# Kernel tuning notes

Hardware: AMD Instinct MI355X
Metric: run time of the kernel (lower is better)

The kernel has to match this reference:

```python
import jax, jax.numpy as jnp
import numpy as np
import math

E = 768      # embed_dim
N = 16       # ssm state_dim
K = 4        # d_conv
R = 48       # dt_rank = ceil(E/16)
DEPTH = 4
V = 32000    # vocab
B = 2
L = 1024
T = 100
H = 4 * E    # mlp hidden


def layer_norm(x, g, b):
    mu = jnp.mean(x, axis=-1, keepdims=True)
    var = jnp.mean(jnp.square(x - mu), axis=-1, keepdims=True)
    return (x - mu) * jax.lax.rsqrt(var + 1e-5) * g + b


def sin_emb(t, dim):
    half = dim // 2
    freqs = jnp.exp(-math.log(10000.0) * jnp.arange(half, dtype=jnp.float32) / half)
    args = t.astype(jnp.float32)[:, None] * freqs
    return jnp.concatenate([jnp.sin(args), jnp.cos(args)], axis=-1)


def ssm_forward(x, z_w, p_w, conv_w, dtp_w, dtp_b, A_log, Dp, out_w):
    # x: (B, L, E)
    z = x @ z_w.T
    params = x @ p_w.T                      # (B, L, R+2N)
    dt_un, _B_unused, Cp = jnp.split(params, [R, R + N], axis=-1)
    dt = jax.nn.softplus(dt_un @ dtp_w.T + dtp_b)   # (B, L, E)
    # depthwise causal conv (torch pads both sides d_conv-1 then trims -> left pad only)
    xc = jax.lax.conv_general_dilated(
        jnp.transpose(x, (0, 2, 1)), conv_w, (1,), [(K - 1, 0)],
        feature_group_count=E, dimension_numbers=('NCH', 'OIH', 'NCH'))
    u = jax.nn.silu(jnp.transpose(xc, (0, 2, 1)))   # (B, L, E)
    A = -jnp.exp(A_log)                              # (E, N)
    A_t = jnp.exp(dt[..., None] * A)                 # (B, L, E, N)
    B_t = jnp.where(jnp.abs(A) < 1e-5, dt[..., None], (A_t - 1.0) / (A + 1e-10))
    # recurrence exactly as source: h[0]=B[0]*u[0]; h[t]=A[t-1]*h[t-1]+B[t-1]*u[t-1]
    h0 = B_t[:, 0] * u[:, 0, :, None]                # (B, E, N)
    xs = (jnp.moveaxis(A_t[:, :-1], 1, 0),
          jnp.moveaxis(B_t[:, :-1], 1, 0),
          jnp.moveaxis(u[:, :-1], 1, 0))
    def step(h, inp):
        a, b, uu = inp
        h = a * h + b * uu[..., None]
        return h, h
    _, hs = jax.lax.scan(step, h0, xs)               # (L-1, B, E, N)
    h_all = jnp.concatenate([h0[None], hs], axis=0)  # (L, B, E, N)
    y = jnp.einsum('bln,lben->ble', Cp, h_all)
    y = y + u * Dp
    return (y * jax.nn.silu(z)) @ out_w.T


def setup_inputs() -> dict:
    key = jax.random.key(0)
    ks = list(jax.random.split(key, 32))
    it = iter(ks)
    def nrm(shape, fan_in):
        return jax.random.normal(next(it), shape, jnp.float32) * np.sqrt(2.0 / fan_in)
    d = {}
    d['tokens'] = jax.random.randint(next(it), (B, L), 0, V + 1)
    d['timesteps'] = jax.random.randint(next(it), (B,), 0, T)
    d['tok_emb'] = jax.random.normal(next(it), (V + 1, E), jnp.float32) * 0.02
    d['time_w1'] = nrm((H, E), E); d['time_b1'] = jnp.zeros((H,), jnp.float32)
    d['time_w2'] = nrm((E, H), H); d['time_b2'] = jnp.zeros((E,), jnp.float32)
    d['ln1_g'] = jnp.ones((DEPTH, E), jnp.float32); d['ln1_b'] = jnp.zeros((DEPTH, E), jnp.float32)
    d['z_w'] = nrm((DEPTH, E, E), E)
    d['p_w'] = nrm((DEPTH, R + 2 * N, E), E)
    d['conv_w'] = jax.random.normal(next(it), (DEPTH, E, 1, K), jnp.float32) * np.sqrt(1.0 / K)
    s = R ** -0.5 * 0.1
    d['dtp_w'] = jax.random.uniform(next(it), (DEPTH, E, R), jnp.float32, -s, s)
    d['dtp_b'] = jnp.full((DEPTH, E), math.log(math.expm1(0.001)), jnp.float32)
    d['A_log'] = jnp.tile(jnp.log(jnp.arange(1, N + 1, dtype=jnp.float32)), (DEPTH, E, 1))
    d['D_param'] = jnp.ones((DEPTH, E), jnp.float32)
    d['out_w'] = nrm((DEPTH, E, E), E)
    d['ln2_g'] = jnp.ones((DEPTH, E), jnp.float32); d['ln2_b'] = jnp.zeros((DEPTH, E), jnp.float32)
    d['mlp_w1'] = nrm((DEPTH, H, E), E); d['mlp_b1'] = jnp.zeros((DEPTH, H), jnp.float32)
    d['mlp_w2'] = nrm((DEPTH, E, H), H); d['mlp_b2'] = jnp.zeros((DEPTH, E), jnp.float32)
    d['lnout_g'] = jnp.ones((E,), jnp.float32); d['lnout_b'] = jnp.zeros((E,), jnp.float32)
    d['head_w'] = nrm((V, E), E); d['head_b'] = jnp.zeros((V,), jnp.float32)
    return d


def reference(tokens, timesteps, tok_emb, time_w1, time_b1, time_w2, time_b2,
              ln1_g, ln1_b, z_w, p_w, conv_w, dtp_w, dtp_b, A_log, D_param, out_w,
              ln2_g, ln2_b, mlp_w1, mlp_b1, mlp_w2, mlp_b2,
              lnout_g, lnout_b, head_w, head_b):
    temb = sin_emb(timesteps, E)
    temb = jax.nn.silu(temb @ time_w1.T + time_b1) @ time_w2.T + time_b2
    x = tok_emb[tokens] + temb[:, None, :]           # (B, L, E)
    for i in range(DEPTH):
        x = x + ssm_forward(layer_norm(x, ln1_g[i], ln1_b[i]),
                            z_w[i], p_w[i], conv_w[i], dtp_w[i], dtp_b[i],
                            A_log[i], D_param[i], out_w[i])
        h = layer_norm(x, ln2_g[i], ln2_b[i])
        h = jax.nn.gelu(h @ mlp_w1[i].T + mlp_b1[i], approximate=False) @ mlp_w2[i].T + mlp_b2[i]
        x = x + h
    x = layer_norm(x, lnout_g, lnout_b)
    return x @ head_w.T + head_b                     # (B, L, V)
```

## Files before the change

kernel.cpp:

```cpp
#include <hip/hip_runtime.h>
#include <math.h>

#define EE 768
#define NS 16
#define RR 48
#define NDEPTH 4
#define NB 2
#define NL 1024
#define NH 3072
#define NV 32000
#define M_ROWS (NB*NL)
#define NC 64
#define CL 16
#define ZPW 896
#define LOG2E 1.44269504088896f
#define LN2   0.69314718055995f

typedef __attribute__((ext_vector_type(8))) __bf16 bf16x8;
typedef __attribute__((ext_vector_type(4))) __bf16 bf16x4;
typedef __attribute__((ext_vector_type(4))) float f32x4;

__device__ __forceinline__ void gl_lds16(const __bf16* g, __bf16* l){
  __builtin_amdgcn_global_load_lds(
      (const __attribute__((address_space(1))) void*)g,
      (__attribute__((address_space(3))) void*)l, 16, 0, 0);
}

enum { BE_STORE=0, BE_BIAS=1, BE_RESID=2, BE_BIAS_RESID=3, BE_BIAS_GELU_B16=4,
       BE_STORE_ZP=5 };

template<int EPI, int BMT, int BNT>
__global__ __launch_bounds__(256) void gemm_bf16(const __bf16* __restrict__ A,
    const __bf16* __restrict__ W, const float* __restrict__ bias,
    void* __restrict__ Cv, float* __restrict__ dtf, float* __restrict__ aux,
    int N, int K, int gx, int gy)
{
  const int nwg = gx*gy;
  const int orig = blockIdx.x;
  const int q = nwg >> 3, r = nwg & 7;
  const int xcd = orig & 7, bse = orig >> 3;
  int wg = (xcd < r ? xcd*(q+1) : r*(q+1) + (xcd-r)*q) + bse;
  const int GN = 16;
  const int per = gy*GN;
  const int g = wg / per;
  const int gstart = g*GN;
  const int gw0 = gx - gstart;
  const int gw = (GN < gw0) ? GN : gw0;
  const int local = wg - g*per;
  const int bx = gstart + local % gw;
  const int by = local / gw;

  constexpr int MFR = BMT/32;
  constexpr int NFR = BNT/32;
  __shared__ __bf16 As[BMT][64];
  __shared__ __bf16 Ws[BNT][64];
  const int bm = by*BMT, bn = bx*BNT;
  const int tid = threadIdx.x;
  const int w = tid>>6, lane = tid&63;
  const int wr = w>>1, wc = w&1;
  const int fr = lane&15, kg = lane>>4;
  const int sr8 = lane>>3;
  const int sg  = lane&7;
  const int ksrc = ((sg ^ sr8) & 7)*8;

  f32x4 acc[MFR][NFR];
  #pragma unroll
  for (int m=0;m<MFR;m++)
    #pragma unroll
    for (int n=0;n<NFR;n++)
      acc[m][n] = (f32x4){0.f,0.f,0.f,0.f};

  for (int k0=0;k0<K;k0+=64){
    const __bf16* gA = A + (size_t)(bm + w*(BMT/4) + sr8)*K + k0 + ksrc;
    #pragma unroll
    for (int c8=0;c8<BMT/32;c8++)
      gl_lds16(gA + (size_t)(c8*8)*K, &As[w*(BMT/4) + c8*8][0]);
    const __bf16* gW = W + (size_t)(bn + w*(BNT/4) + sr8)*K + k0 + ksrc;
    #pragma unroll
    for (int c8=0;c8<BNT/32;c8++)
      gl_lds16(gW + (size_t)(c8*8)*K, &Ws[w*(BNT/4) + c8*8][0]);
    __syncthreads();
    #pragma unroll
    for (int kk=0;kk<2;kk++){
      const int sp = (((kg + kk*4) ^ (fr&7)) & 7) * 8;
      bf16x8 af[MFR], bfr[NFR];
      #pragma unroll
      for (int m=0;m<MFR;m++) af[m]  = *(const bf16x8*)&As[wr*(BMT/2) + m*16 + fr][sp];
      #pragma unroll
      for (int n=0;n<NFR;n++) bfr[n] = *(const bf16x8*)&Ws[wc*(BNT/2) + n*16 + fr][sp];
      #pragma unroll
      for (int m=0;m<MFR;m++)
        #pragma unroll
        for (int n=0;n<NFR;n++)
          acc[m][n] = __builtin_amdgcn_mfma_f32_16x16x32_bf16(af[m], bfr[n], acc[m][n], 0,0,0);
    }
    __syncthreads();
  }

  float* Cf = (float*)Cv;
  __bf16* Cb = (__bf16*)Cv;
  #pragma unroll
  for (int m=0;m<MFR;m++){
    int row = bm + wr*(BMT/2) + m*16 + kg*4;
    #pragma unroll
    for (int n=0;n<NFR;n++){
      int col = bn + wc*(BNT/2) + n*16 + fr;
      float bsv = 0.f;
      if (EPI==BE_BIAS || EPI==BE_BIAS_RESID || EPI==BE_BIAS_GELU_B16)
        bsv = bias[col];
      #pragma unroll
      for (int rr2=0;rr2<4;rr2++){
        float v = acc[m][n][rr2];
        size_t idx = (size_t)(row+rr2)*N + col;
        if (EPI==BE_STORE)            Cf[idx] = v;
        else if (EPI==BE_BIAS)        Cf[idx] = v + bsv;
        else if (EPI==BE_RESID)       Cf[idx] += v;
        else if (EPI==BE_BIAS_RESID)  Cf[idx] += v + bsv;
        else if (EPI==BE_BIAS_GELU_B16){
          float xg = v + bsv; Cb[idx] = (__bf16)(0.5f*xg*(1.f+erff(xg*0.70710678118654752f)));
        } else if (EPI==BE_STORE_ZP){
          if (col < 768)                    Cb[(size_t)(row+rr2)*EE + col] = (__bf16)v;
          else if (col < 816)               dtf[(size_t)(row+rr2)*RR + (col-768)] = v;
          else if (col >= 832 && col < 848) aux[(size_t)(row+rr2)*16 + (col-832)] = v;
        }
      }
    }
  }
}

__global__ __launch_bounds__(512) void gemm_head256(const __bf16* __restrict__ A,
    const __bf16* __restrict__ W, const float* __restrict__ bias,
    float* __restrict__ C)
{
  const int gx = NV/256, gy = M_ROWS/256;
  const int nwg = gx*gy;
  const int orig = blockIdx.x;
  const int q = nwg >> 3;
  const int xcd = orig & 7, bse = orig >> 3;
  int wg = xcd*q + bse;
  const int GN = 8;
  const int per = gy*GN;
  const int g = wg / per;
  const int gstart = g*GN;
  const int gw0 = gx - gstart;
  const int gw = (GN < gw0) ? GN : gw0;
  const int local = wg - g*per;
  const int bx = gstart + local % gw;
  const int by = local / gw;

  __shared__ __bf16 Ah[2][256][64];
  __shared__ __bf16 Wh[2][256][64];
  const int bm = by*256, bn = bx*256;
  const int tid = threadIdx.x;
  const int w = tid>>6, lane = tid&63;
  const int wr = w>>2, wc = w&3;
  const int fr = lane&15, kg = lane>>4;
  const int ksrc = (((lane&7) ^ ((lane>>3)&7)) & 7)*8;

  f32x4 acc[8][4];
  #pragma unroll
  for (int m=0;m<8;m++)
    #pragma unroll
    for (int n=0;n<4;n++)
      acc[m][n] = (f32x4){0.f,0.f,0.f,0.f};

  auto stage = [&](int bufp, int kt){
    const __bf16* gA = A + (size_t)(bm + w*8 + (lane>>3))*EE + kt*64 + ksrc;
    #pragma unroll
    for (int j=0;j<4;j++)
      gl_lds16(gA + (size_t)(j*64)*EE, &Ah[bufp][j*64 + w*8][0]);
    const __bf16* gW = W + (size_t)(bn + w*8 + (lane>>3))*EE + kt*64 + ksrc;
    #pragma unroll
    for (int j=0;j<4;j++)
      gl_lds16(gW + (size_t)(j*64)*EE, &Wh[bufp][j*64 + w*8][0]);
  };

  auto compute = [&](int bufp){
    bf16x8 bfr[4][2];
    #pragma unroll
    for (int kk=0;kk<2;kk++){
      const int sp = (((kg + kk*4) ^ (fr&7)) & 7) * 8;
      #pragma unroll
      for (int n=0;n<4;n++)
        bfr[n][kk] = *(const bf16x8*)&Wh[bufp][wc*64 + n*16 + fr][sp];
    }
    #pragma unroll
    for (int m=0;m<8;m++){
      const int arow = wr*128 + m*16 + fr;
      const int sp0 = ((kg ^ (fr&7)) & 7) * 8;
      const int sp1 = (((kg+4) ^ (fr&7)) & 7) * 8;
      bf16x8 a0 = *(const bf16x8*)&Ah[bufp][arow][sp0];
      bf16x8 a1 = *(const bf16x8*)&Ah[bufp][arow][sp1];
      #pragma unroll
      for (int n=0;n<4;n++){
        acc[m][n] = __builtin_amdgcn_mfma_f32_16x16x32_bf16(a0, bfr[n][0], acc[m][n], 0,0,0);
        acc[m][n] = __builtin_amdgcn_mfma_f32_16x16x32_bf16(a1, bfr[n][1], acc[m][n], 0,0,0);
      }
    }
  };

  stage(0, 0);
  __syncthreads();
  for (int kt=0; kt<12; kt+=2){
    stage(1, kt+1);
    compute(0);
    __syncthreads();
    if (kt+2 < 12) stage(0, kt+2);
    compute(1);
    __syncthreads();
  }

  #pragma unroll
  for (int m=0;m<8;m++){
    int row = bm + wr*128 + m*16 + kg*4;
    #pragma unroll
    for (int n=0;n<4;n++){
      int col = bn + wc*64 + n*16 + fr;
      float bsv = bias[col];
      #pragma unroll
      for (int rr2=0;rr2<4;rr2++)
        C[(size_t)(row+rr2)*NV + col] = acc[m][n][rr2] + bsv;
    }
  }
}

#define S1E 2752512LL
#define S2E 5111808LL
#define S3E 14548992LL
#define S4E 23986176LL
#define STOT 48562176LL

__global__ void f2b_all(const float* __restrict__ zw, const float* __restrict__ pw,
                        const float* __restrict__ ow, const float* __restrict__ m1,
                        const float* __restrict__ m2, const float* __restrict__ hw,
                        __bf16* __restrict__ o){
  long long idx = ((long long)blockIdx.x*256 + threadIdx.x)*4;
  if (idx >= STOT) return;
  float4 v;
  if (idx < S1E){
    long long layer = idx / (ZPW*EE);
    int rem = (int)(idx - layer*(ZPW*EE));
    int row = rem / EE, col = rem - (rem/EE)*EE;
    if (row < 768)      v = *(const float4*)(zw + ((size_t)layer*EE + row)*EE + col);
    else if (row < 848) v = *(const float4*)(pw + ((size_t)layer*80 + (row-768))*EE + col);
    else                v = make_float4(0.f,0.f,0.f,0.f);
  }
  else if (idx < S2E) v = *(const float4*)(ow + (idx - S1E));
  else if (idx < S3E) v = *(const float4*)(m1 + (idx - S2E));
  else if (idx < S4E) v = *(const float4*)(m2 + (idx - S3E));
  else                v = *(const float4*)(hw + (idx - S4E));
  bf16x4 rb = { (__bf16)v.x, (__bf16)v.y, (__bf16)v.z, (__bf16)v.w };
  *(bf16x4*)(o+idx) = rb;
}

__global__ __launch_bounds__(256) void ln_kernel(const float* __restrict__ x,
    const float* __restrict__ gp, const float* __restrict__ bp, __bf16* __restrict__ yb)
{
  int row = blockIdx.x*4 + (threadIdx.x>>6);
  int lane = threadIdx.x & 63;
  const float* xr = x + (size_t)row*EE;
  float4 v0 = *(const float4*)(xr + lane*4);
  float4 v1 = *(const float4*)(xr + 256 + lane*4);
  float4 v2 = *(const float4*)(xr + 512 + lane*4);
  float s = (v0.x+v0.y)+(v0.z+v0.w) + (v1.x+v1.y)+(v1.z+v1.w) + (v2.x+v2.y)+(v2.z+v2.w);
  float q = v0.x*v0.x+v0.y*v0.y+v0.z*v0.z+v0.w*v0.w
          + v1.x*v1.x+v1.y*v1.y+v1.z*v1.z+v1.w*v1.w
          + v2.x*v2.x+v2.y*v2.y+v2.z*v2.z+v2.w*v2.w;
  #pragma unroll
  for (int m=1;m<64;m<<=1){ s += __shfl_xor(s, m, 64); q += __shfl_xor(q, m, 64); }
  float mu  = s*(1.f/768.f);
  float var = q*(1.f/768.f) - mu*mu;
  float inv = 1.0f/sqrtf(var + 1e-5f);
  __bf16* ybr = yb + (size_t)row*EE;
  #pragma unroll
  for (int p=0;p<3;p++){
    const float4 v = (p==0)? v0 : (p==1)? v1 : v2;
    int o = p*256 + lane*4;
    float4 gg = *(const float4*)(gp + o);
    float4 bb = *(const float4*)(bp + o);
    bf16x4 ov = { (__bf16)((v.x-mu)*inv*gg.x + bb.x),
                  (__bf16)((v.y-mu)*inv*gg.y + bb.y),
                  (__bf16)((v.z-mu)*inv*gg.z + bb.z),
                  (__bf16)((v.w-mu)*inv*gg.w + bb.w) };
    *(bf16x4*)(ybr + o) = ov;
  }
}

__global__ void sinemb_kernel(const int* __restrict__ timesteps, float* __restrict__ emb){
  int i = blockIdx.x*256+threadIdx.x;
  if (i >= NB*EE) return;
  int b = i/EE, e = i - b*EE;
  int half = EE/2;
  int j = (e<half)? e : e-half;
  float freq = expf(-logf(10000.f)*(float)j/(float)half);
  float arg = (float)timesteps[b]*freq;
  emb[i] = (e<half)? sinf(arg) : cosf(arg);
}

__global__ void time_mlp1(const float* __restrict__ emb, const float* __restrict__ w1,
                          const float* __restrict__ b1, float* __restrict__ thid){
  int wid = (blockIdx.x*256 + threadIdx.x)>>6;
  int lane = threadIdx.x & 63;
  int b = wid / NH, h = wid - b*NH;
  const float* er = emb + b*EE;
  const float* wr = w1 + (size_t)h*EE;
  float s = 0.f;
  #pragma unroll
  for (int j=0;j<EE/64;j++) s = fmaf(er[j*64+lane], wr[j*64+lane], s);
  #pragma unroll
  for (int m=1;m<64;m<<=1) s += __shfl_xor(s, m, 64);
  if (lane==0){
    s += b1[h];
    thid[wid] = s/(1.f+expf(-s));
  }
}

__global__ void time_mlp2(const float* __restrict__ thid, const float* __restrict__ w2,
                          const float* __restrict__ b2, float* __restrict__ temb){
  int wid = (blockIdx.x*256 + threadIdx.x)>>6;
  int lane = threadIdx.x & 63;
  int b = wid / EE, e = wid - b*EE;
  const float* tr = thid + b*NH;
  const float* wr = w2 + (size_t)e*NH;
  float s = 0.f;
  #pragma unroll
  for (int j=0;j<NH/64;j++) s = fmaf(tr[j*64+lane], wr[j*64+lane], s);
  #pragma unroll
  for (int m=1;m<64;m<<=1) s += __shfl_xor(s, m, 64);
  if (lane==0) temb[wid] = s + b2[e];
}

__global__ void embed_kernel(const int* __restrict__ tokens, const float* __restrict__ tok_emb,
                             const float* __restrict__ temb, float* __restrict__ x){
  int idx = blockIdx.x*256+threadIdx.x;
  int e = idx % EE; int bl = idx / EE; int b = bl / NL;
  int tok = tokens[bl];
  x[idx] = tok_emb[(size_t)tok*EE + e] + temb[b*EE + e];
}

__device__ __forceinline__ float dot48(const float* __restrict__ row, const float* wdf){
  float a0=0.f,a1=0.f,a2=0.f,a3=0.f;
  #pragma unroll
  for (int j=0;j<12;j++){
    float4 v = *(const float4*)(row + j*4);
    a0 = fmaf(v.x, wdf[j*4+0], a0);
    a1 = fmaf(v.y, wdf[j*4+1], a1);
    a2 = fmaf(v.z, wdf[j*4+2], a2);
    a3 = fmaf(v.w, wdf[j*4+3], a3);
  }
  return (a0+a1)+(a2+a3);
}
__device__ __forceinline__ float softplus_f(float x){
  return fmaxf(x,0.f) + LN2*log2f(1.f + exp2f(-LOG2E*fabsf(x)));
}
__device__ __forceinline__ float silu_f(float x){
  return x/(1.f + exp2f(-LOG2E*x));
}

__global__ __launch_bounds__(256) void scan_fused(
    const __bf16* __restrict__ xnb, const float* __restrict__ dtun,
    const float* __restrict__ dtw, const float* __restrict__ dtbias,
    const float* __restrict__ cwp, const float* __restrict__ A_log,
    const float* __restrict__ Dp, const float* __restrict__ cpf,
    const __bf16* __restrict__ zgb, __bf16* __restrict__ gb)
{
  __shared__ float Pl[NC][4][NS];
  __shared__ float Sl[NC][4][NS];
  __shared__ float dtc_l[CL][256];
  __shared__ float uc_l[CL+1][256];
  const int tid = threadIdx.x;
  const int e_l = tid & 3, c = tid >> 2;
  const int b  = blockIdx.x / (EE/4);
  const int eg = blockIdx.x % (EE/4);
  const int e  = eg*4 + e_l;

  float wdf[48];
  #pragma unroll
  for (int j=0;j<12;j++){
    float4 v = *(const float4*)(dtw + (size_t)e*RR + j*4);
    wdf[j*4]=v.x; wdf[j*4+1]=v.y; wdf[j*4+2]=v.z; wdf[j*4+3]=v.w;
  }
  float4 cw = *(const float4*)(cwp + e*4);
  float bias = dtbias[e];
  float Dv = Dp[e];
  float Av2[NS], iAv[NS];
  #pragma unroll
  for (int n4=0;n4<4;n4++){
    float4 v = *(const float4*)(A_log + (size_t)e*NS + n4*4);
    float a0=-exp2f(LOG2E*v.x), a1=-exp2f(LOG2E*v.y), a2=-exp2f(LOG2E*v.z), a3=-exp2f(LOG2E*v.w);
    Av2[n4*4+0]=a0*LOG2E; Av2[n4*4+1]=a1*LOG2E; Av2[n4*4+2]=a2*LOG2E; Av2[n4*4+3]=a3*LOG2E;
    iAv[n4*4+0]=1.f/(a0+1e-10f); iAv[n4*4+1]=1.f/(a1+1e-10f);
    iAv[n4*4+2]=1.f/(a2+1e-10f); iAv[n4*4+3]=1.f/(a3+1e-10f);
  }
  const __bf16* xcol = xnb + (size_t)b*NL*EE + e;
  const float* dtrow0 = dtun + (size_t)b*NL*RR;
  const int cs = c*CL;

  {
    float xw0,xw1,xw2,xw3;
    int prow = (c==0)? 0 : cs-1;
    xw0 = (prow-3>=0)? (float)xcol[(size_t)(prow-3)*EE] : 0.f;
    xw1 = (prow-2>=0)? (float)xcol[(size_t)(prow-2)*EE] : 0.f;
    xw2 = (prow-1>=0)? (float)xcol[(size_t)(prow-1)*EE] : 0.f;
    xw3 = (float)xcol[(size_t)prow*EE];
    float up  = silu_f(cw.x*xw0 + cw.y*xw1 + cw.z*xw2 + cw.w*xw3);
    float dtp_ = softplus_f(dot48(dtrow0 + (size_t)prow*RR, wdf) + bias);
    float h[NS];
    float sumdt = 0.f;
    #pragma unroll
    for (int n=0;n<NS;n++) h[n]=0.f;
    for (int i=0;i<CL;i++){
      int tt = cs+i;
      bool z0 = (tt==0);
      dtc_l[i][tid] = dtp_;
      uc_l[i][tid]  = up;
      sumdt += dtp_;
      #pragma unroll
      for (int n=0;n<NS;n++){
        float at = exp2f(dtp_*Av2[n]);
        float bt = (at-1.f)*iAv[n];
        float s = bt*up;
        h[n] = z0 ? s : fmaf(at, h[n], s);
      }
      if (tt>0){
        xw0=xw1; xw1=xw2; xw2=xw3; xw3 = (float)xcol[(size_t)tt*EE];
        up  = silu_f(cw.x*xw0 + cw.y*xw1 + cw.z*xw2 + cw.w*xw3);
        dtp_ = softplus_f(dot48(dtrow0 + (size_t)tt*RR, wdf) + bias);
      }
    }
    uc_l[CL][tid] = up;
    #pragma unroll
    for (int n4=0;n4<4;n4++){
      float4 pv;
      if (c==0) pv = make_float4(0.f,0.f,0.f,0.f);
      else pv = make_float4(exp2f(Av2[n4*4+0]*sumdt), exp2f(Av2[n4*4+1]*sumdt),
                            exp2f(Av2[n4*4+2]*sumdt), exp2f(Av2[n4*4+3]*sumdt));
      *(float4*)&Pl[c][e_l][n4*4] = pv;
      *(float4*)&Sl[c][e_l][n4*4] = make_float4(h[n4*4],h[n4*4+1],h[n4*4+2],h[n4*4+3]);
    }
  }
  __syncthreads();
  if (tid < 64){
    int el2 = tid & 3, n = tid >> 2;
    float hh = 0.f;
    for (int cc=0; cc<NC; cc++){
      float pp = Pl[cc][el2][n], ss = Sl[cc][el2][n];
      Pl[cc][el2][n] = hh;
      hh = fmaf(pp, hh, ss);
    }
  }
  __syncthreads();
  {
    float h[NS];
    #pragma unroll
    for (int n4=0;n4<4;n4++){
      float4 v = *(const float4*)&Pl[c][e_l][n4*4];
      h[n4*4]=v.x; h[n4*4+1]=v.y; h[n4*4+2]=v.z; h[n4*4+3]=v.w;
    }
    #pragma unroll
    for (int i=0;i<CL;i++){
      int tt = cs+i;
      bool z0 = (tt==0);
      float dtp_ = dtc_l[i][tid];
      float up   = uc_l[i][tid];
      float ucur = uc_l[i+1][tid];
      #pragma unroll
      for (int n=0;n<NS;n++){
        float at = exp2f(dtp_*Av2[n]);
        float bt = (at-1.f)*iAv[n];
        float s = bt*up;
        h[n] = z0 ? s : fmaf(at, h[n], s);
      }
      const float* cpr = cpf + (size_t)(b*NL+tt)*16;
      float y = 0.f;
      #pragma unroll
      for (int n4=0;n4<4;n4++){
        float4 cv = *(const float4*)(cpr + n4*4);
        y = fmaf(cv.x, h[n4*4], y);   y = fmaf(cv.y, h[n4*4+1], y);
        y = fmaf(cv.z, h[n4*4+2], y); y = fmaf(cv.w, h[n4*4+3], y);
      }
      float zv = (float)zgb[(size_t)(b*NL+tt)*EE + e];
      gb[(size_t)(b*NL+tt)*EE + e] = (__bf16)((y + ucur*Dv)*silu_f(zv));
    }
  }
}

extern "C" void kernel_launch(void* const* d_in, const int* in_sizes, int n_in,
                              void* d_out, int out_size, void* d_ws, size_t ws_size,
                              hipStream_t stream) {
  const int*   tokens    = (const int*)d_in[0];
  const int*   timesteps = (const int*)d_in[1];
  const float* tok_emb   = (const float*)d_in[2];
  const float* time_w1   = (const float*)d_in[3];
  const float* time_b1   = (const float*)d_in[4];
  const float* time_w2   = (const float*)d_in[5];
  const float* time_b2   = (const float*)d_in[6];
  const float* ln1_g     = (const float*)d_in[7];
  const float* ln1_b     = (const float*)d_in[8];
  const float* z_w       = (const float*)d_in[9];
  const float* p_w       = (const float*)d_in[10];
  const float* conv_w    = (const float*)d_in[11];
  const float* dtp_w     = (const float*)d_in[12];
  const float* dtp_b     = (const float*)d_in[13];
  const float* A_log     = (const float*)d_in[14];
  const float* D_param   = (const float*)d_in[15];
  const float* out_w     = (const float*)d_in[16];
  const float* ln2_g     = (const float*)d_in[17];
  const float* ln2_b     = (const float*)d_in[18];
  const float* mlp_w1    = (const float*)d_in[19];
  const float* mlp_b1    = (const float*)d_in[20];
  const float* mlp_w2    = (const float*)d_in[21];
  const float* mlp_b2    = (const float*)d_in[22];
  const float* lnout_g   = (const float*)d_in[23];
  const float* lnout_b   = (const float*)d_in[24];
  const float* head_w    = (const float*)d_in[25];
  const float* head_b    = (const float*)d_in[26];
  float* out = (float*)d_out;

  float* ws = (float*)d_ws;
  float* x      = ws;
  float* cpf    = x    + (size_t)M_ROWS*EE;
  float* dtun   = cpf  + (size_t)M_ROWS*16;
  float* emb    = dtun + (size_t)M_ROWS*RR;
  float* thid   = emb + NB*EE;
  __bf16* xnb   = (__bf16*)(thid + NB*NH);
  __bf16* zgb   = xnb + (size_t)M_ROWS*EE;
  __bf16* gb    = zgb + (size_t)M_ROWS*EE;
  __bf16* hidb  = gb  + (size_t)M_ROWS*EE;
  __bf16* wzp   = hidb + (size_t)M_ROWS*NH;
  __bf16* wout  = wzp  + (size_t)NDEPTH*ZPW*EE;
  __bf16* wm1   = wout + (size_t)NDEPTH*EE*EE;
  __bf16* wm2   = wm1  + (size_t)NDEPTH*NH*EE;
  __bf16* whead = wm2  + (size_t)NDEPTH*EE*NH;

  f2b_all<<<(int)(STOT/4/256), 256, 0, stream>>>(z_w, p_w, out_w, mlp_w1, mlp_w2, head_w, wzp);

  sinemb_kernel<<<(NB*EE+255)/256, 256, 0, stream>>>(timesteps, emb);
  time_mlp1<<<NB*NH/4, 256, 0, stream>>>(emb, time_w1, time_b1, thid);
  time_mlp2<<<NB*EE/4, 256, 0, stream>>>(thid, time_w2, time_b2, emb);
  embed_kernel<<<M_ROWS*EE/256, 256, 0, stream>>>(tokens, tok_emb, emb, x);

  const int scan_grid = NB*EE/4;

  for (int i=0;i<NDEPTH;i++){
    const float* dtw = dtp_w + (size_t)i*EE*RR;
    const float* dtb = dtp_b + i*EE;
    const float* cwp = conv_w + (size_t)i*EE*4;
    const float* al  = A_log + (size_t)i*EE*NS;
    ln_kernel<<<M_ROWS/4, 256, 0, stream>>>(x, ln1_g + i*EE, ln1_b + i*EE, xnb);
    gemm_bf16<BE_STORE_ZP,64,64><<<14*32, 256, 0, stream>>>(
        xnb, wzp + (size_t)i*ZPW*EE, nullptr, zgb, dtun, cpf, ZPW, EE, 14, 32);
    scan_fused<<<scan_grid, 256, 0, stream>>>(xnb, dtun, dtw, dtb, cwp, al,
        D_param + i*EE, cpf, zgb, gb);
    gemm_bf16<BE_RESID,64,64><<<12*32, 256, 0, stream>>>(
        gb, wout + (size_t)i*EE*EE, nullptr, x, nullptr, nullptr, EE, EE, 12, 32);
    ln_kernel<<<M_ROWS/4, 256, 0, stream>>>(x, ln2_g + i*EE, ln2_b + i*EE, xnb);
    gemm_bf16<BE_BIAS_GELU_B16,64,128><<<24*32, 256, 0, stream>>>(
        xnb, wm1 + (size_t)i*NH*EE, mlp_b1 + i*NH, hidb, nullptr, nullptr, NH, EE, 24, 32);
    gemm_bf16<BE_BIAS_RESID,64,64><<<12*32, 256, 0, stream>>>(
        hidb, wm2 + (size_t)i*EE*NH, mlp_b2 + i*EE, x, nullptr, nullptr, EE, NH, 12, 32);
  }
  ln_kernel<<<M_ROWS/4, 256, 0, stream>>>(x, lnout_g, lnout_b, xnb);
  gemm_head256<<<(NV/256)*(M_ROWS/256), 512, 0, stream>>>(xnb, whead, head_b, out);
}
```

Before: 808.3 us.

## Rework head GEMM into 256x128 tiles with triple-buffered LDS pipeline

The vocabulary head GEMM moves from 256x256 tiles with a double-buffered LDS loop to 256x128 tiles with three LDS stages, prefetching two k-tiles ahead. It uses explicit s_waitcnt vmcnt plus s_barrier so each iteration waits only for the oldest stage instead of a full __syncthreads. Each wave now owns a 64x64 sub-tile with fewer accumulators, which lowers register pressure and doubles the number of workgroups. In exchange, A data is re-read more often because output tiles are narrower, and the hand-written wait counts must match the number of loads issued per stage.

```diff
diff --git a/kernel.cpp b/kernel.cpp
--- a/kernel.cpp
+++ b/kernel.cpp
@@ -128,17 +128,17 @@
   }
 }
 
-__global__ __launch_bounds__(512) void gemm_head256(const __bf16* __restrict__ A,
+__global__ __launch_bounds__(512) void gemm_head3p(const __bf16* __restrict__ A,
     const __bf16* __restrict__ W, const float* __restrict__ bias,
     float* __restrict__ C)
 {
-  const int gx = NV/256, gy = M_ROWS/256;
+  const int gx = NV/128, gy = M_ROWS/256;
   const int nwg = gx*gy;
   const int orig = blockIdx.x;
   const int q = nwg >> 3;
   const int xcd = orig & 7, bse = orig >> 3;
   int wg = xcd*q + bse;
-  const int GN = 8;
+  const int GN = 32;
   const int per = gy*GN;
   const int g = wg / per;
   const int gstart = g*GN;
@@ -148,18 +148,18 @@
   const int bx = gstart + local % gw;
   const int by = local / gw;
 
-  __shared__ __bf16 Ah[2][256][64];
-  __shared__ __bf16 Wh[2][256][64];
-  const int bm = by*256, bn = bx*256;
+  __shared__ __bf16 Ah[3][256][64];
+  __shared__ __bf16 Wh[3][128][64];
+  const int bm = by*256, bn = bx*128;
   const int tid = threadIdx.x;
   const int w = tid>>6, lane = tid&63;
-  const int wr = w>>2, wc = w&3;
+  const int wr = w>>1, wc = w&1;
   const int fr = lane&15, kg = lane>>4;
   const int ksrc = (((lane&7) ^ ((lane>>3)&7)) & 7)*8;
 
-  f32x4 acc[8][4];
-  #pragma unroll
-  for (int m=0;m<8;m++)
+  f32x4 acc[4][4];
+  #pragma unroll
+  for (int m=0;m<4;m++)
     #pragma unroll
     for (int n=0;n<4;n++)
       acc[m][n] = (f32x4){0.f,0.f,0.f,0.f};
@@ -171,48 +171,37 @@
       gl_lds16(gA + (size_t)(j*64)*EE, &Ah[bufp][j*64 + w*8][0]);
     const __bf16* gW = W + (size_t)(bn + w*8 + (lane>>3))*EE + kt*64 + ksrc;
     #pragma unroll
-    for (int j=0;j<4;j++)
+    for (int j=0;j<2;j++)
       gl_lds16(gW + (size_t)(j*64)*EE, &Wh[bufp][j*64 + w*8][0]);
   };
 
-  auto compute = [&](int bufp){
-    bf16x8 bfr[4][2];
+  stage(0, 0);
+  stage(1, 1);
+  #pragma unroll
+  for (int t=0;t<12;t++){
+    if (t < 11) asm volatile("s_waitcnt vmcnt(6)\n\ts_barrier" ::: "memory");
+    else        asm volatile("s_waitcnt vmcnt(0)\n\ts_barrier" ::: "memory");
+    const int b_ = t % 3;
     #pragma unroll
     for (int kk=0;kk<2;kk++){
       const int sp = (((kg + kk*4) ^ (fr&7)) & 7) * 8;
-      #pragma unroll
-      for (int n=0;n<4;n++)
-        bfr[n][kk] = *(const bf16x8*)&Wh[bufp][wc*64 + n*16 + fr][sp];
-    }
-    #pragma unroll
-    for (int m=0;m<8;m++){
-      const int arow = wr*128 + m*16 + fr;
-      const int sp0 = ((kg ^ (fr&7)) & 7) * 8;
-      const int sp1 = (((kg+4) ^ (fr&7)) & 7) * 8;
-      bf16x8 a0 = *(const bf16x8*)&Ah[bufp][arow][sp0];
-      bf16x8 a1 = *(const bf16x8*)&Ah[bufp][arow][sp1];
-      #pragma unroll
-      for (int n=0;n<4;n++){
-        acc[m][n] = __builtin_amdgcn_mfma_f32_16x16x32_bf16(a0, bfr[n][0], acc[m][n], 0,0,0);
-        acc[m][n] = __builtin_amdgcn_mfma_f32_16x16x32_bf16(a1, bfr[n][1], acc[m][n], 0,0,0);
-      }
-    }
-  };
-
-  stage(0, 0);
-  __syncthreads();
-  for (int kt=0; kt<12; kt+=2){
-    stage(1, kt+1);
-    compute(0);
-    __syncthreads();
-    if (kt+2 < 12) stage(0, kt+2);
-    compute(1);
-    __syncthreads();
-  }
-
-  #pragma unroll
-  for (int m=0;m<8;m++){
-    int row = bm + wr*128 + m*16 + kg*4;
+      bf16x8 af[4], bfr[4];
+      #pragma unroll
+      for (int m=0;m<4;m++) af[m]  = *(const bf16x8*)&Ah[b_][wr*64 + m*16 + fr][sp];
+      #pragma unroll
+      for (int n=0;n<4;n++) bfr[n] = *(const bf16x8*)&Wh[b_][wc*64 + n*16 + fr][sp];
+      #pragma unroll
+      for (int m=0;m<4;m++)
+        #pragma unroll
+        for (int n=0;n<4;n++)
+          acc[m][n] = __builtin_amdgcn_mfma_f32_16x16x32_bf16(af[m], bfr[n], acc[m][n], 0,0,0);
+    }
+    if (t+2 < 12) stage((t+2)%3, t+2);
+  }
+
+  #pragma unroll
+  for (int m=0;m<4;m++){
+    int row = bm + wr*64 + m*16 + kg*4;
     #pragma unroll
     for (int n=0;n<4;n++){
       int col = bn + wc*64 + n*16 + fr;
@@ -561,5 +550,5 @@
         hidb, wm2 + (size_t)i*EE*NH, mlp_b2 + i*EE, x, nullptr, nullptr, EE, NH, 12, 32);
   }
   ln_kernel<<<M_ROWS/4, 256, 0, stream>>>(x, lnout_g, lnout_b, xnb);
-  gemm_head256<<<(NV/256)*(M_ROWS/256), 512, 0, stream>>>(xnb, whead, head_b, out);
-}
+  gemm_head3p<<<(NV/128)*(M_ROWS/256), 512, 0, stream>>>(xnb, whead, head_b, out);
+}
```

Measured after the change: 775.4 us. 1.04x faster.
